# Optimization experiments

Measured on AMD Instinct MI355X. Metric: run time of the kernel, lower is better.

## Reference

```python
import jax, jax.numpy as jnp
import numpy as np
import math

OBS_DIM = 128
LATENT_DIM = 256
ACT_DIM = 32
BATCH = 262144
MAX_ACTION = 1.0
MEAN_MIN, MEAN_MAX = -7.0, 7.0
LOGSTD_MIN, LOGSTD_MAX = -2.0, 5.0
EPS = 1e-6
LOG_2PI = math.log(2.0 * math.pi)


def setup_inputs() -> dict:
    key = jax.random.key(0)
    ks = jax.random.split(key, 8)
    obs = jax.random.normal(ks[0], (BATCH, OBS_DIM), dtype=jnp.float32)
    noise = jax.random.normal(ks[1], (BATCH, ACT_DIM), dtype=jnp.float32)
    # backbone: Linear(OBS_DIM, LATENT_DIM) + ReLU
    W_bb = jax.random.normal(ks[2], (OBS_DIM, LATENT_DIM), dtype=jnp.float32) * 0.05
    b_bb = jnp.zeros((LATENT_DIM,), dtype=jnp.float32)
    # mu / sigma heads, init uniform(-0.001, 0.001) as in the torch module
    W_mu = jax.random.uniform(ks[3], (LATENT_DIM, ACT_DIM), minval=-0.001, maxval=0.001, dtype=jnp.float32)
    b_mu = jax.random.uniform(ks[4], (ACT_DIM,), minval=-0.001, maxval=0.001, dtype=jnp.float32)
    W_sigma = jax.random.uniform(ks[5], (LATENT_DIM, ACT_DIM), minval=-0.001, maxval=0.001, dtype=jnp.float32)
    b_sigma = jax.random.uniform(ks[6], (ACT_DIM,), minval=-0.001, maxval=0.001, dtype=jnp.float32)
    return {"obs": obs, "noise": noise, "W_bb": W_bb, "b_bb": b_bb,
            "W_mu": W_mu, "b_mu": b_mu, "W_sigma": W_sigma, "b_sigma": b_sigma}


def reference(obs, noise, W_bb, b_bb, W_mu, b_mu, W_sigma, b_sigma):
    # backbone
    h = jax.nn.relu(obs @ W_bb + b_bb)                      # [B, L]
    mu = jnp.clip(h @ W_mu + b_mu, MEAN_MIN, MEAN_MAX)      # [B, A]
    logstd = jnp.clip(h @ W_sigma + b_sigma, LOGSTD_MIN, LOGSTD_MAX)
    std = jnp.exp(logstd)
    # NOTE: torch code passes diag_embed(std) as COVARIANCE -> scale = sqrt(std)
    pretanh = mu + jnp.sqrt(std) * noise                    # rsample
    action = MAX_ACTION * jnp.tanh(pretanh)
    # MVN(mu, diag(std)) log-prob, diagonal closed form (no NxN matrix)
    d = mu.shape[-1]
    pretanh_log_prob = (-0.5 * jnp.sum((pretanh - mu) ** 2 / std + logstd, axis=-1)
                        - 0.5 * d * LOG_2PI)                # [B]
    log_prob = pretanh_log_prob - jnp.sum(jnp.log(1.0 - action ** 2 + EPS), axis=-1)
    return (action, pretanh, log_prob, pretanh_log_prob)
```

## Files before the change

### kernel.cpp

```cpp
#include <hip/hip_runtime.h>
#include <hip/hip_bf16.h>


#define B_TOTAL 262144
#define OBS_D   128
#define LAT     256
#define ACT     32

typedef __attribute__((ext_vector_type(8))) short bf16x8;
typedef __attribute__((ext_vector_type(4))) float f32x4;

__device__ __forceinline__ unsigned short f2bf(float x) {
  __hip_bfloat16 h = __float2bfloat16(x);
  return __builtin_bit_cast(unsigned short, h);
}

__device__ __forceinline__ float ftanh(float x) {
  float ax = fabsf(x);
  float e  = __expf(-2.f * ax);
  float y  = (1.f - e) / (1.f + e);
  return x < 0.f ? -y : y;
}

__global__ void dice_prep(const float* __restrict__ Wbb,
                          const float* __restrict__ Wmu,
                          const float* __restrict__ Wsg,
                          unsigned short* __restrict__ wpack) {
  int tid = blockIdx.x * 256 + threadIdx.x;
  if (tid < 32768) {
    int w    = tid >> 13;
    int rem  = tid & 8191;
    int f    = rem >> 9;
    int lane = (rem >> 3) & 63;
    int j    = rem & 7;
    int t = f >> 2, s = f & 3;
    int k = s * 32 + (lane >> 4) * 8 + j;
    int n = w * 64 + t * 16 + (lane & 15);
    wpack[tid] = f2bf(Wbb[k * LAT + n]);
  } else {
    int i    = tid - 32768;
    int f    = i >> 9;
    int lane = (i >> 3) & 63;
    int j    = i & 7;
    int s = f >> 2, u = f & 3;
    int n = u * 16 + (lane & 15);
    int k = s * 32 + (lane >> 4) * 8 + j;
    float v = (n < 32) ? Wmu[k * ACT + n] : Wsg[k * ACT + (n - 32)];
    wpack[32768 + i] = f2bf(v);
  }
}

__global__ __launch_bounds__(256, 2) void dice_main(
    const float* __restrict__ obs, const float* __restrict__ noise,
    const unsigned short* __restrict__ wpack,
    const float* __restrict__ b_bb, const float* __restrict__ b_mu,
    const float* __restrict__ b_sg, float* __restrict__ out) {

  __shared__ __align__(16) unsigned char s_obs[8192];
  __shared__ __align__(16) unsigned char s_h[32768];

  const int tid  = threadIdx.x;
  const int wave = tid >> 6, lane = tid & 63;
  const int lrow = lane & 15, lgrp = lane >> 4;
  const int blockRow0 = blockIdx.x * 64;

  bf16x8 wf[16];
  {
    const bf16x8* wp = (const bf16x8*)wpack + wave * 1024 + lane;
#pragma unroll
    for (int f = 0; f < 16; ++f) wf[f] = wp[f * 64];
  }

  float bbias[4];
#pragma unroll
  for (int t = 0; t < 4; ++t) bbias[t] = b_bb[wave * 64 + t * 16 + lrow];

  auto stage_obs = [&](int half) {
    const float4* op = (const float4*)obs + (size_t)(blockRow0 + half * 32) * 32;
#pragma unroll
    for (int i = 0; i < 4; ++i) {
      int flat = i * 256 + tid;
      int m = flat >> 5, kq = flat & 31;
      float4 v = op[m * 32 + kq];
      unsigned int lo = (unsigned int)f2bf(v.x) | ((unsigned int)f2bf(v.y) << 16);
      unsigned int hi = (unsigned int)f2bf(v.z) | ((unsigned int)f2bf(v.w) << 16);
      int byte = m * 256 + ((kq * 8) ^ ((m & 15) << 4));
      *(uint2*)(s_obs + byte) = make_uint2(lo, hi);
    }
  };

  auto backbone = [&](int st) {
    const int m0 = st * 16, mloc = (st & 1) * 16;
    bf16x8 a[4];
#pragma unroll
    for (int s = 0; s < 4; ++s) {
      int abyte = (mloc + lrow) * 256 + ((s * 64 + lgrp * 16) ^ (lrow << 4));
      a[s] = *(const bf16x8*)(s_obs + abyte);
    }
    f32x4 acc[4];
#pragma unroll
    for (int t = 0; t < 4; ++t) acc[t] = (f32x4)(0.f);
#pragma unroll
    for (int t = 0; t < 4; ++t)
#pragma unroll
      for (int s = 0; s < 4; ++s)
        acc[t] = __builtin_amdgcn_mfma_f32_16x16x32_bf16(a[s], wf[t * 4 + s], acc[t], 0, 0, 0);
#pragma unroll
    for (int t = 0; t < 4; ++t) {
      int col = wave * 64 + t * 16 + lrow;
#pragma unroll
      for (int r = 0; r < 4; ++r) {
        int row = m0 + lgrp * 4 + r;
        float v = fmaxf(acc[t][r] + bbias[t], 0.f);
        int byte = row * 512 + ((2 * col) ^ ((row & 15) << 4));
        *(unsigned short*)(s_h + byte) = f2bf(v);
      }
    }
  };

  stage_obs(0);
  __syncthreads();
  backbone(0);
  backbone(1);
  __syncthreads();
  stage_obs(1);
  __syncthreads();
  backbone(2);
  backbone(3);
  __syncthreads();

  const bf16x8* hb = (const bf16x8*)(wpack + 32768);
  f32x4 acc2[4];
#pragma unroll
  for (int u = 0; u < 4; ++u) acc2[u] = (f32x4)(0.f);
#pragma unroll
  for (int s = 0; s < 8; ++s) {
    int off = (s * 64 + lgrp * 16) ^ (lrow << 4);
    bf16x8 a = *(const bf16x8*)(s_h + (wave * 16 + lrow) * 512 + off);
#pragma unroll
    for (int u = 0; u < 4; ++u) {
      bf16x8 b = hb[(s * 4 + u) * 64 + lane];
      acc2[u] = __builtin_amdgcn_mfma_f32_16x16x32_bf16(a, b, acc2[u], 0, 0, 0);
    }
  }

  const float bmu0 = b_mu[lrow], bmu1 = b_mu[lrow + 16];
  const float bsg0 = b_sg[lrow], bsg1 = b_sg[lrow + 16];
  float* out_act = out;
  float* out_pre = out + (B_TOTAL * ACT);
  float* out_lp  = out + (2 * B_TOTAL * ACT);
  float* out_plp = out_lp + B_TOTAL;

  float s1v[4], s2v[4];
#pragma unroll
  for (int r = 0; r < 4; ++r) {
    int row = blockRow0 + wave * 16 + lgrp * 4 + r;
    float mu0 = fminf(fmaxf(acc2[0][r] + bmu0, -7.f), 7.f);
    float mu1 = fminf(fmaxf(acc2[1][r] + bmu1, -7.f), 7.f);
    float ls0 = fminf(fmaxf(acc2[2][r] + bsg0, -2.f), 5.f);
    float ls1 = fminf(fmaxf(acc2[3][r] + bsg1, -2.f), 5.f);
    float n0 = noise[row * ACT + lrow];
    float n1 = noise[row * ACT + lrow + 16];
    float sp0 = __expf(0.5f * ls0), sp1 = __expf(0.5f * ls1);
    float p0 = fmaf(sp0, n0, mu0), p1 = fmaf(sp1, n1, mu1);
    float a0 = ftanh(p0), a1 = ftanh(p1);
    float d0 = p0 - mu0, d1 = p1 - mu1;
    float t1 = fmaf(d0 * d0, __expf(-ls0), ls0) + fmaf(d1 * d1, __expf(-ls1), ls1);
    float t2 = __logf(1.f - a0 * a0 + 1e-6f) + __logf(1.f - a1 * a1 + 1e-6f);
    out_act[row * ACT + lrow]      = a0;
    out_act[row * ACT + lrow + 16] = a1;
    out_pre[row * ACT + lrow]      = p0;
    out_pre[row * ACT + lrow + 16] = p1;
    s1v[r] = t1;
    s2v[r] = t2;
  }
#pragma unroll
  for (int m = 1; m < 16; m <<= 1) {
#pragma unroll
    for (int r = 0; r < 4; ++r) {
      s1v[r] += __shfl_xor(s1v[r], m, 64);
      s2v[r] += __shfl_xor(s2v[r], m, 64);
    }
  }
  if (lrow < 4) {
    int r = lrow;
    float s1 = (r == 0) ? s1v[0] : (r == 1) ? s1v[1] : (r == 2) ? s1v[2] : s1v[3];
    float s2 = (r == 0) ? s2v[0] : (r == 1) ? s2v[1] : (r == 2) ? s2v[2] : s2v[3];
    int row = blockRow0 + wave * 16 + lgrp * 4 + r;
    float plp = -0.5f * s1 - 29.406033062549525f;
    out_plp[row] = plp;
    out_lp[row]  = plp - s2;
  }
}

extern "C" void kernel_launch(void* const* d_in, const int* in_sizes, int n_in,
                              void* d_out, int out_size, void* d_ws, size_t ws_size,
                              hipStream_t stream) {
  const float* obs = (const float*)d_in[0];
  const float* noi = (const float*)d_in[1];
  const float* Wbb = (const float*)d_in[2];
  const float* bbb = (const float*)d_in[3];
  const float* Wmu = (const float*)d_in[4];
  const float* bmu = (const float*)d_in[5];
  const float* Wsg = (const float*)d_in[6];
  const float* bsg = (const float*)d_in[7];
  unsigned short* wpack = (unsigned short*)d_ws;

  hipLaunchKernelGGL(dice_prep, dim3(192), dim3(256), 0, stream, Wbb, Wmu, Wsg, wpack);
  hipLaunchKernelGGL(dice_main, dim3(B_TOTAL / 64), dim3(256), 0, stream,
                     obs, noi, wpack, bbb, bmu, bsg, (float*)d_out);
}
```

Before: 63.78 us.

## Load obs directly into MFMA registers, drop obs LDS staging and syncs

Each wave now reads its obs rows straight from global memory into bf16 MFMA A-fragments, replacing the cooperative LDS staging buffer and three barriers. Freeing the 8 KB obs buffer lets launch bounds ask for 4 blocks per CU to raise occupancy. The trade-off is that all four waves now load the same obs rows redundantly (4x global/L2 reads of obs), with less coalesced 32-byte per-lane accesses. The tighter register budget may also force spills of the 16 preloaded weight fragments.

```diff
diff --git a/kernel.cpp b/kernel.cpp
--- a/kernel.cpp
+++ b/kernel.cpp
@@ -50,13 +50,12 @@
   }
 }
 
-__global__ __launch_bounds__(256, 2) void dice_main(
+__global__ __launch_bounds__(256, 4) void dice_main(
     const float* __restrict__ obs, const float* __restrict__ noise,
     const unsigned short* __restrict__ wpack,
     const float* __restrict__ b_bb, const float* __restrict__ b_mu,
     const float* __restrict__ b_sg, float* __restrict__ out) {
 
-  __shared__ __align__(16) unsigned char s_obs[8192];
   __shared__ __align__(16) unsigned char s_h[32768];
 
   const int tid  = threadIdx.x;
@@ -75,27 +74,20 @@
 #pragma unroll
   for (int t = 0; t < 4; ++t) bbias[t] = b_bb[wave * 64 + t * 16 + lrow];
 
-  auto stage_obs = [&](int half) {
-    const float4* op = (const float4*)obs + (size_t)(blockRow0 + half * 32) * 32;
 #pragma unroll
-    for (int i = 0; i < 4; ++i) {
-      int flat = i * 256 + tid;
-      int m = flat >> 5, kq = flat & 31;
-      float4 v = op[m * 32 + kq];
-      unsigned int lo = (unsigned int)f2bf(v.x) | ((unsigned int)f2bf(v.y) << 16);
-      unsigned int hi = (unsigned int)f2bf(v.z) | ((unsigned int)f2bf(v.w) << 16);
-      int byte = m * 256 + ((kq * 8) ^ ((m & 15) << 4));
-      *(uint2*)(s_obs + byte) = make_uint2(lo, hi);
-    }
-  };
-
-  auto backbone = [&](int st) {
-    const int m0 = st * 16, mloc = (st & 1) * 16;
+  for (int st = 0; st < 4; ++st) {
+    const float* ap = obs + (size_t)(blockRow0 + st * 16 + lrow) * OBS_D + lgrp * 8;
     bf16x8 a[4];
 #pragma unroll
     for (int s = 0; s < 4; ++s) {
-      int abyte = (mloc + lrow) * 256 + ((s * 64 + lgrp * 16) ^ (lrow << 4));
-      a[s] = *(const bf16x8*)(s_obs + abyte);
+      float4 v0 = *(const float4*)(ap + s * 32);
+      float4 v1 = *(const float4*)(ap + s * 32 + 4);
+      bf16x8 t;
+      t[0] = (short)f2bf(v0.x); t[1] = (short)f2bf(v0.y);
+      t[2] = (short)f2bf(v0.z); t[3] = (short)f2bf(v0.w);
+      t[4] = (short)f2bf(v1.x); t[5] = (short)f2bf(v1.y);
+      t[6] = (short)f2bf(v1.z); t[7] = (short)f2bf(v1.w);
+      a[s] = t;
     }
     f32x4 acc[4];
 #pragma unroll
@@ -110,23 +102,14 @@
       int col = wave * 64 + t * 16 + lrow;
 #pragma unroll
       for (int r = 0; r < 4; ++r) {
-        int row = m0 + lgrp * 4 + r;
+        int row = st * 16 + lgrp * 4 + r;
         float v = fmaxf(acc[t][r] + bbias[t], 0.f);
         int byte = row * 512 + ((2 * col) ^ ((row & 15) << 4));
         *(unsigned short*)(s_h + byte) = f2bf(v);
       }
     }
-  };
+  }
 
-  stage_obs(0);
-  __syncthreads();
-  backbone(0);
-  backbone(1);
-  __syncthreads();
-  stage_obs(1);
-  __syncthreads();
-  backbone(2);
-  backbone(3);
   __syncthreads();
 
   const bf16x8* hb = (const bf16x8*)(wpack + 32768);
```

Result: slower. 113.1 us (+77.4%).
